# Performance work log

Measured on AMD Instinct MI355X. Metric: run time of the kernel, lower is better.

Reference implementation:

```python
import jax, jax.numpy as jnp
import numpy as np

HID = 128
N_NODES = 50000
N_REL = 500
N_EDGES = 625000
BN_EPS = 1e-5
LRELU_SLOPE = 0.01


def _xavier(key, shape):
    fan_in, fan_out = shape[1], shape[0]
    std = float(np.sqrt(2.0 / (fan_in + fan_out)))
    return jax.random.normal(key, shape, dtype=jnp.float32) * std


def setup_inputs() -> dict:
    key = jax.random.key(0)
    ks = jax.random.split(key, 16)
    x = jax.random.normal(ks[0], (N_NODES, HID), dtype=jnp.float32)
    r = jax.random.normal(ks[1], (N_REL, HID), dtype=jnp.float32)
    que_context = jax.random.normal(ks[2], (1, HID), dtype=jnp.float32)
    fin_que = jax.random.normal(ks[3], (1, 1, HID), dtype=jnp.float32)
    edge_index = jax.random.randint(ks[4], (2, N_EDGES), 0, N_NODES, dtype=jnp.int64)
    edge_attr = jax.random.randint(ks[5], (N_EDGES,), 0, N_REL, dtype=jnp.int64)
    return {
        "x": x, "r": r, "que_context": que_context, "fin_que": fin_que,
        "edge_index": edge_index, "edge_attr": edge_attr,
        # mess_comp: Linear(2*hid, hid) + Tanh
        "W_mess": _xavier(ks[6], (HID, 2 * HID)), "b_mess": jnp.zeros((HID,), jnp.float32),
        # mess_atten_trans: Linear(2*hid, hid) + LeakyReLU
        "W_matt": _xavier(ks[7], (HID, 2 * HID)), "b_matt": jnp.zeros((HID,), jnp.float32),
        "mess_atten_weight": _xavier(ks[8], (1, HID)),
        # x_atten_trans: Linear(2*hid, hid) + LeakyReLU
        "W_xatt": _xavier(ks[9], (HID, 2 * HID)), "b_xatt": jnp.zeros((HID,), jnp.float32),
        "x_atten_weight": _xavier(ks[10], (1, HID)),
        # BatchNorm1d(hid) affine params (training-mode batch stats are used)
        "bn_gamma": jnp.ones((HID,), jnp.float32), "bn_beta": jnp.zeros((HID,), jnp.float32),
    }


def reference(x, r, que_context, fin_que, edge_index, edge_attr,
              W_mess, b_mess, W_matt, b_matt, mess_atten_weight,
              W_xatt, b_xatt, x_atten_weight, bn_gamma, bn_beta):
    n_nodes = x.shape[0]
    # BatchNorm1d over relation embeddings (training-mode: batch statistics, biased var)
    mu = jnp.mean(r, axis=0)
    var = jnp.mean(jnp.square(r - mu), axis=0)
    r = (r - mu) * jax.lax.rsqrt(var + BN_EPS) * bn_gamma + bn_beta

    head_ents, tail_ents = edge_index[0], edge_index[1]
    head_embeds = x[head_ents]            # [E, H]
    rel_embeds = r[edge_attr]             # [E, H]

    # message computation: Linear(2H->H) + tanh
    mess_in = jnp.concatenate([head_embeds, rel_embeds], axis=1)  # [E, 2H]
    mess = jnp.tanh(mess_in @ W_mess.T + b_mess)                  # [E, H]

    # message attention logits
    qc = jnp.broadcast_to(que_context, (mess.shape[0], que_context.shape[1]))
    mc = jnp.concatenate([mess, qc], axis=1) @ W_matt.T + b_matt
    mc = jax.nn.leaky_relu(mc, LRELU_SLOPE)
    mess_coeffs = jnp.sum(mess_atten_weight * mc, axis=1)         # [E]

    # segment softmax over tail_ents
    seg_max = jax.ops.segment_max(mess_coeffs, tail_ents, num_segments=n_nodes)
    mess_coeffs = jnp.exp(mess_coeffs - seg_max[tail_ents])
    seg_sum = jax.ops.segment_sum(mess_coeffs, tail_ents, num_segments=n_nodes)
    mess_weights = mess_coeffs / (seg_sum[tail_ents] + 1e-16)

    # weighted scatter-sum aggregation
    sum_mess = jax.ops.segment_sum(mess * mess_weights[:, None], tail_ents,
                                   num_segments=n_nodes)          # [N, H]

    # gating attention between x and aggregated messages
    pair = jnp.stack([x, sum_mess], axis=1)                       # [N, 2, H]
    fq = jnp.broadcast_to(fin_que, (n_nodes, 2, fin_que.shape[2]))
    xc = jnp.concatenate([pair, fq], axis=2)                      # [N, 2, 2H]
    xc = jax.nn.leaky_relu(jnp.einsum('nkc,hc->nkh', xc, W_xatt) + b_xatt, LRELU_SLOPE)
    x_coeffs = jnp.sum(x_atten_weight[None] * xc, axis=2)         # [N, 2]
    x_weight = jax.nn.softmax(x_coeffs, axis=1)
    x_out = x_weight[:, 0:1] * x + x_weight[:, 1:2] * sum_mess
    # dropout is identity (eval / p=0)
    return x_out, r
```

## Files before the change

kernel.cpp:

```cpp
#include <hip/hip_runtime.h>
#include <hip/hip_bf16.h>

#define HID 128
#define NN 50000
#define NR 500
#define NE 625000
#define LRELU 0.01f
#define SCAN_BLOCKS 196

typedef __hip_bfloat16 bf16;
typedef __attribute__((ext_vector_type(8))) short short8;
typedef __attribute__((ext_vector_type(4))) float float4_;

__device__ __forceinline__ float b2f(bf16 v) { return __bfloat162float(v); }
__device__ __forceinline__ bf16 f2b(float v) { return __float2bfloat16(v); }

__device__ __forceinline__ float san(float v) {
    return (v == v && v > -1e30f && v < 1e30f) ? v : 0.f;
}

__device__ __forceinline__ float ftanh(float a) {
    float e = __expf(2.f * a);
    return 1.f - 2.f * __builtin_amdgcn_rcpf(e + 1.f);
}

__device__ __forceinline__ float ldf(const void* p, int i, int f32) {
    return f32 ? ((const float*)p)[i] : b2f(((const bf16*)p)[i]);
}
__device__ __forceinline__ void stf(void* p, int i, float v, int f32) {
    if (f32) ((float*)p)[i] = v;
    else ((bf16*)p)[i] = f2b(v);
}

__device__ __forceinline__ int clampi(int v, int hi) {
    return v < 0 ? 0 : (v >= hi ? hi - 1 : v);
}
__device__ __forceinline__ int idx_at(const int* p, int i, int is64) {
    return p[is64 ? (2 * i) : i];
}

__device__ __forceinline__ unsigned short bfbits(float v) {
    bf16 h = f2b(v);
    return *(unsigned short*)&h;
}
__device__ __forceinline__ unsigned int packbf2(float a, float b) {
    return (unsigned int)bfbits(a) | ((unsigned int)bfbits(b) << 16);
}
__device__ __forceinline__ float bflo(unsigned int u) { return __uint_as_float(u << 16); }
__device__ __forceinline__ float bfhi(unsigned int u) { return __uint_as_float(u & 0xffff0000u); }

__device__ __forceinline__ float xorReduce16(float v) {
    v += __shfl_xor(v, 1, 64);
    v += __shfl_xor(v, 2, 64);
    v += __shfl_xor(v, 4, 64);
    v += __shfl_xor(v, 8, 64);
    return v;
}
__device__ __forceinline__ float waveMax(float v) {
#pragma unroll
    for (int o = 1; o < 64; o <<= 1) v = fmaxf(v, __shfl_xor(v, o, 64));
    return v;
}
__device__ __forceinline__ float waveSum(float v) {
#pragma unroll
    for (int o = 1; o < 64; o <<= 1) v += __shfl_xor(v, o, 64);
    return v;
}

struct DetectArr {
    const void* p[16];
    int sz[16];
    int kind[16];
};

__global__ void detect_all(DetectArr d, int* __restrict__ flags) {
    int b = blockIdx.x;
    if (d.kind[b] == 1) {
        if (threadIdx.x == 0) {
            const int* q = (const int*)d.p[b];
            int o = 0;
            for (int i = 0; i < 64; ++i) o |= q[2 * i + 1];
            flags[b] = (o == 0) ? 1 : 0;
        }
        return;
    }
    __shared__ int sb[64], sf[64];
    const unsigned int* w = (const unsigned int*)d.p[b];
    int K = d.sz[b] >> 1;
    if (K > 4096) K = 4096;
    int bv = 0, fv = 0;
    for (int i = threadIdx.x; i < K; i += 64) {
        unsigned int x = w[i];
        unsigned int lo = x & 0xFFFFu, hi = x >> 16;
        if (lo == 0u) {
            if (hi) fv++;
        } else {
            unsigned int e = (lo >> 7) & 0xFFu;
            if (e >= 90u && e <= 160u) bv++;
            else fv++;
        }
    }
    sb[threadIdx.x] = bv; sf[threadIdx.x] = fv;
    __syncthreads();
    if (threadIdx.x == 0) {
        int B = 0, F = 0;
        for (int i = 0; i < 64; ++i) { B += sb[i]; F += sf[i]; }
        flags[b] = (F > B) ? 1 : 0;
    }
}

__global__ void bn_stats(const void* __restrict__ r, const int* __restrict__ flags,
                         float* __restrict__ stats) {
    __shared__ float sb[256], sq[256];
    const int fr = flags[1];
    int h = blockIdx.x;
    int t = threadIdx.x;
    float s = 0.f, ss = 0.f;
    for (int i = t; i < NR; i += 256) {
        float v = ldf(r, i * HID + h, fr);
        s += v; ss += v * v;
    }
    sb[t] = s; sq[t] = ss;
    __syncthreads();
    for (int o = 128; o > 0; o >>= 1) {
        if (t < o) { sb[t] += sb[t + o]; sq[t] += sq[t + o]; }
        __syncthreads();
    }
    if (t == 0) {
        float mu = sb[0] / NR;
        float var = sq[0] / NR - mu * mu;
        if (var < 0.f) var = 0.f;
        stats[h] = mu;
        stats[HID + h] = rsqrtf(var + 1e-5f);
    }
}

__global__ void bn_apply(const void* __restrict__ r, const void* __restrict__ gamma,
                         const void* __restrict__ beta, const int* __restrict__ flags,
                         const float* __restrict__ stats,
                         float* __restrict__ rnorm, void* __restrict__ out_base) {
    const int fr = flags[1], fg = flags[14], fb = flags[15], fo = flags[0];
    int i = blockIdx.x * 256 + threadIdx.x;
    if (i >= NR * HID) return;
    int h = i & 127;
    float v = san((ldf(r, i, fr) - stats[h]) * stats[HID + h] * ldf(gamma, h, fg)
                  + ldf(beta, h, fb));
    rnorm[i] = v;
    stf(out_base, NN * HID + i, v, fo);
}

__global__ void precomp_kernel(const void* __restrict__ Wmatt, const void* __restrict__ bmatt,
                               const void* __restrict__ qc,
                               const void* __restrict__ Wxatt, const void* __restrict__ bxatt,
                               const void* __restrict__ fq, const int* __restrict__ flags,
                               float* __restrict__ cmatt, float* __restrict__ cxatt) {
    __shared__ float qcs[HID], fqs[HID];
    const int fWm = flags[8], fbm = flags[9], fqc = flags[2];
    const int fWx = flags[11], fbx = flags[12], ffq = flags[3];
    int h = threadIdx.x;
    qcs[h] = ldf(qc, h, fqc);
    fqs[h] = ldf(fq, h, ffq);
    __syncthreads();
    float a = ldf(bmatt, h, fbm), b = ldf(bxatt, h, fbx);
    for (int k = 0; k < HID; ++k) {
        a += ldf(Wmatt, h * 2 * HID + HID + k, fWm) * qcs[k];
        b += ldf(Wxatt, h * 2 * HID + HID + k, fWx) * fqs[k];
    }
    cmatt[h] = san(a);
    cxatt[h] = san(b);
}

__global__ void rm_kernel(const void* __restrict__ Wmess, const void* __restrict__ bmess,
                          const int* __restrict__ flags,
                          const float* __restrict__ rnorm, bf16* __restrict__ Rmb) {
    __shared__ float rl[HID];
    const int fW = flags[6], fb = flags[7];
    int rel = blockIdx.x, h = threadIdx.x;
    rl[h] = rnorm[rel * HID + h];
    __syncthreads();
    float a = ldf(bmess, h, fb);
    for (int k = 0; k < HID; ++k)
        a += ldf(Wmess, h * 2 * HID + HID + k, fW) * rl[k];
    Rmb[rel * HID + h] = f2b(san(a));
}

#define MLDA 136

__device__ __forceinline__ short8 load_bfrag(const void* W, int n, int k0, int f32) {
    short8 b;
    if (f32) {
        const float* Wf = (const float*)W + (size_t)n * 2 * HID + k0;
        float4 u0 = *(const float4*)Wf;
        float4 u1 = *(const float4*)(Wf + 4);
        b[0] = (short)bfbits(u0.x); b[1] = (short)bfbits(u0.y);
        b[2] = (short)bfbits(u0.z); b[3] = (short)bfbits(u0.w);
        b[4] = (short)bfbits(u1.x); b[5] = (short)bfbits(u1.y);
        b[6] = (short)bfbits(u1.z); b[7] = (short)bfbits(u1.w);
    } else {
        b = *(const short8*)((const bf16*)W + (size_t)n * 2 * HID + k0);
    }
    return b;
}

__global__ __launch_bounds__(256, 4) void xm_mfma(const void* __restrict__ x,
                                                  const void* __restrict__ Wmess,
                                                  const int* __restrict__ flags,
                                                  bf16* __restrict__ Xmb) {
    __shared__ short ml[64 * MLDA];
    const int fx = flags[0], fW = flags[6];
    int tid = threadIdx.x;
    int l = tid & 63, w = tid >> 6;
    int quad = l >> 4, lo16 = l & 15;
    int nbase = w * 32;
    short8 bfr[2][4];
#pragma unroll
    for (int nt = 0; nt < 2; ++nt)
#pragma unroll
        for (int kk = 0; kk < 4; ++kk)
            bfr[nt][kk] = load_bfrag(Wmess, nbase + nt * 16 + lo16, kk * 32 + quad * 8, fW);

    const int ntiles = (NN + 63) / 64;
    for (int tile = blockIdx.x; tile < ntiles; tile += gridDim.x) {
        __syncthreads();
#pragma unroll
        for (int p = 0; p < 8; ++p) {
            int rl_ = p * 8 + (tid >> 5);
            int node = clampi(tile * 64 + rl_, NN);
            int k4 = (tid & 31) * 4;
            unsigned int o0, o1;
            if (fx) {
                float4 v = *(const float4*)((const float*)x + (size_t)node * HID + k4);
                o0 = packbf2(v.x, v.y);
                o1 = packbf2(v.z, v.w);
            } else {
                uint2 u = *(const uint2*)((const bf16*)x + (size_t)node * HID + k4);
                o0 = u.x; o1 = u.y;
            }
            unsigned int* dst = (unsigned int*)&ml[rl_ * MLDA + k4];
            dst[0] = o0; dst[1] = o1;
        }
        __syncthreads();
        float4_ acc[4][2];
#pragma unroll
        for (int mt = 0; mt < 4; ++mt)
#pragma unroll
            for (int nt = 0; nt < 2; ++nt)
                acc[mt][nt] = (float4_){0.f, 0.f, 0.f, 0.f};
#pragma unroll
        for (int kk = 0; kk < 4; ++kk) {
            short8 a[4];
#pragma unroll
            for (int mt = 0; mt < 4; ++mt)
                a[mt] = *(const short8*)&ml[(mt * 16 + lo16) * MLDA + kk * 32 + quad * 8];
#pragma unroll
            for (int mt = 0; mt < 4; ++mt)
#pragma unroll
                for (int nt = 0; nt < 2; ++nt)
                    acc[mt][nt] = __builtin_amdgcn_mfma_f32_16x16x32_bf16(
                        a[mt], bfr[nt][kk], acc[mt][nt], 0, 0, 0);
        }
#pragma unroll
        for (int mt = 0; mt < 4; ++mt)
#pragma unroll
            for (int nt = 0; nt < 2; ++nt)
#pragma unroll
                for (int r = 0; r < 4; ++r) {
                    int node = tile * 64 + mt * 16 + quad * 4 + r;
                    if (node < NN)
                        Xmb[node * HID + nbase + nt * 16 + lo16] = f2b(san(acc[mt][nt][r]));
                }
    }
}

__global__ __launch_bounds__(256, 6) void edge_coeff_mfma(
        const bf16* __restrict__ Xmb, const bf16* __restrict__ Rmb,
        const void* __restrict__ Wmatt, const float* __restrict__ cmatt,
        const void* __restrict__ maw, const unsigned int* __restrict__ hrcsr,
        const int* __restrict__ flags, float* __restrict__ ccsr) {
    __shared__ short ml[64 * MLDA];
    __shared__ float swave[4][64];
    const int fWm = flags[8], fmw = flags[10];
    int tid = threadIdx.x;
    int l = tid & 63, w = tid >> 6;
    int quad = l >> 4, lo16 = l & 15;
    int nbase = w * 32;
    short8 bfr[2][4];
#pragma unroll
    for (int nt = 0; nt < 2; ++nt)
#pragma unroll
        for (int kk = 0; kk < 4; ++kk)
            bfr[nt][kk] = load_bfrag(Wmatt, nbase + nt * 16 + lo16, kk * 32 + quad * 8, fWm);

    int n0 = nbase + lo16, n1 = n0 + 16;
    float c0 = cmatt[n0], c1 = cmatt[n1];
    float w0 = ldf(maw, n0, fmw), w1 = ldf(maw, n1, fmw);

    const int ntiles = (NE + 63) / 64;
    const int seg = tid & 15;
    const int rowsub = tid >> 4;
    for (int T = blockIdx.x; T < ntiles; T += gridDim.x) {
        __syncthreads();
#pragma unroll
        for (int p = 0; p < 4; ++p) {
            int el = p * 16 + rowsub;
            int slot = T * 64 + el;
            unsigned int hr = hrcsr[slot < NE ? slot : NE - 1];
            int head = hr & 0xffffu, rel = hr >> 16;
            int k8 = seg * 8;
            uint4 xv = *(const uint4*)&Xmb[head * HID + k8];
            uint4 rv = *(const uint4*)&Rmb[rel * HID + k8];
            uint4 o;
            o.x = packbf2(ftanh(bflo(xv.x) + bflo(rv.x)), ftanh(bfhi(xv.x) + bfhi(rv.x)));
            o.y = packbf2(ftanh(bflo(xv.y) + bflo(rv.y)), ftanh(bfhi(xv.y) + bfhi(rv.y)));
            o.z = packbf2(ftanh(bflo(xv.z) + bflo(rv.z)), ftanh(bfhi(xv.z) + bfhi(rv.z)));
            o.w = packbf2(ftanh(bflo(xv.w) + bflo(rv.w)), ftanh(bfhi(xv.w) + bfhi(rv.w)));
            *(uint4*)&ml[el * MLDA + k8] = o;
        }
        __syncthreads();
        float4_ acc[4][2];
#pragma unroll
        for (int mt = 0; mt < 4; ++mt)
#pragma unroll
            for (int nt = 0; nt < 2; ++nt)
                acc[mt][nt] = (float4_){0.f, 0.f, 0.f, 0.f};
#pragma unroll
        for (int kk = 0; kk < 4; ++kk) {
            short8 a[4];
#pragma unroll
            for (int mt = 0; mt < 4; ++mt)
                a[mt] = *(const short8*)&ml[(mt * 16 + lo16) * MLDA + kk * 32 + quad * 8];
#pragma unroll
            for (int mt = 0; mt < 4; ++mt)
#pragma unroll
                for (int nt = 0; nt < 2; ++nt)
                    acc[mt][nt] = __builtin_amdgcn_mfma_f32_16x16x32_bf16(
                        a[mt], bfr[nt][kk], acc[mt][nt], 0, 0, 0);
        }
#pragma unroll
        for (int mt = 0; mt < 4; ++mt)
#pragma unroll
            for (int r = 0; r < 4; ++r) {
                float z0 = acc[mt][0][r] + c0;
                z0 = z0 > 0.f ? z0 : LRELU * z0;
                float z1 = acc[mt][1][r] + c1;
                z1 = z1 > 0.f ? z1 : LRELU * z1;
                float s = w0 * z0 + w1 * z1;
                s = xorReduce16(s);
                if (lo16 == 0) swave[w][mt * 16 + quad * 4 + r] = s;
            }
        __syncthreads();
        if (tid < 64) {
            int slot = T * 64 + tid;
            if (slot < NE)
                ccsr[slot] = san(swave[0][tid] + swave[1][tid] + swave[2][tid] + swave[3][tid]);
        }
    }
}

__global__ __launch_bounds__(256, 4) void gate_mfma(
        const void* __restrict__ x, const bf16* __restrict__ smb,
        const void* __restrict__ Wxatt, const float* __restrict__ cxatt,
        const void* __restrict__ xaw, const int* __restrict__ flags,
        void* __restrict__ outx) {
    __shared__ short ml[64 * MLDA];
    __shared__ float swave[4][64];
    __shared__ float lgL[64];
    const int fx = flags[0], fWx = flags[11], fxw = flags[13], fo = flags[0];
    int tid = threadIdx.x;
    int l = tid & 63, w = tid >> 6;
    int quad = l >> 4, lo16 = l & 15;
    int nbase = w * 32;
    short8 bfr[2][4];
#pragma unroll
    for (int nt = 0; nt < 2; ++nt)
#pragma unroll
        for (int kk = 0; kk < 4; ++kk)
            bfr[nt][kk] = load_bfrag(Wxatt, nbase + nt * 16 + lo16, kk * 32 + quad * 8, fWx);

    int n0 = nbase + lo16, n1 = n0 + 16;
    float c0 = cxatt[n0], c1 = cxatt[n1];
    float w0 = ldf(xaw, n0, fxw), w1 = ldf(xaw, n1, fxw);

    const int ntiles = (NN + 31) / 32;
    for (int tile = blockIdx.x; tile < ntiles; tile += gridDim.x) {
        __syncthreads();
#pragma unroll
        for (int p = 0; p < 8; ++p) {
            int rl_ = p * 8 + (tid >> 5);
            int node = clampi(tile * 32 + (rl_ >> 1), NN);
            int k4 = (tid & 31) * 4;
            unsigned int o0, o1;
            if (rl_ & 1) {
                uint2 u = *(const uint2*)&smb[node * HID + k4];
                o0 = u.x; o1 = u.y;
            } else if (fx) {
                float4 v = *(const float4*)((const float*)x + (size_t)node * HID + k4);
                o0 = packbf2(v.x, v.y);
                o1 = packbf2(v.z, v.w);
            } else {
                uint2 u = *(const uint2*)((const bf16*)x + (size_t)node * HID + k4);
                o0 = u.x; o1 = u.y;
            }
            unsigned int* dst = (unsigned int*)&ml[rl_ * MLDA + k4];
            dst[0] = o0; dst[1] = o1;
        }
        __syncthreads();
        float4_ acc[4][2];
#pragma unroll
        for (int mt = 0; mt < 4; ++mt)
#pragma unroll
            for (int nt = 0; nt < 2; ++nt)
                acc[mt][nt] = (float4_){0.f, 0.f, 0.f, 0.f};
#pragma unroll
        for (int kk = 0; kk < 4; ++kk) {
            short8 a[4];
#pragma unroll
            for (int mt = 0; mt < 4; ++mt)
                a[mt] = *(const short8*)&ml[(mt * 16 + lo16) * MLDA + kk * 32 + quad * 8];
#pragma unroll
            for (int mt = 0; mt < 4; ++mt)
#pragma unroll
                for (int nt = 0; nt < 2; ++nt)
                    acc[mt][nt] = __builtin_amdgcn_mfma_f32_16x16x32_bf16(
                        a[mt], bfr[nt][kk], acc[mt][nt], 0, 0, 0);
        }
#pragma unroll
        for (int mt = 0; mt < 4; ++mt)
#pragma unroll
            for (int r = 0; r < 4; ++r) {
                float z0 = acc[mt][0][r] + c0;
                z0 = z0 > 0.f ? z0 : LRELU * z0;
                float z1 = acc[mt][1][r] + c1;
                z1 = z1 > 0.f ? z1 : LRELU * z1;
                float s = w0 * z0 + w1 * z1;
                s = xorReduce16(s);
                if (lo16 == 0) swave[w][mt * 16 + quad * 4 + r] = s;
            }
        __syncthreads();
        if (tid < 64)
            lgL[tid] = san(swave[0][tid] + swave[1][tid] + swave[2][tid] + swave[3][tid]);
        __syncthreads();
#pragma unroll
        for (int it = 0; it < 16; ++it) {
            int idx = tid + 256 * it;
            int nl = idx >> 7, h = idx & 127;
            int node = tile * 32 + nl;
            if (node < NN) {
                float g0 = lgL[2 * nl], g1 = lgL[2 * nl + 1];
                float mm = fmaxf(g0, g1);
                float e0 = __expf(g0 - mm), e1 = __expf(g1 - mm);
                float inv = __builtin_amdgcn_rcpf(e0 + e1);
                float xv = ldf(x, node * HID + h, fx);
                float sv = b2f(smb[node * HID + h]);
                stf(outx, node * HID + h, san((e0 * xv + e1 * sv) * inv), fo);
            }
        }
    }
}

__global__ void count_kernel(const int* __restrict__ ei, const int* __restrict__ flags,
                             int* __restrict__ counts) {
    const int is64e = flags[4];
    for (int e = blockIdx.x * blockDim.x + threadIdx.x; e < NE; e += gridDim.x * blockDim.x) {
        int tail = clampi(idx_at(ei, NE + e, is64e), NN);
        atomicAdd(&counts[tail], 1);
    }
}

__global__ void scan_phase1(const int* __restrict__ counts, int* __restrict__ offs,
                            int* __restrict__ bsum) {
    __shared__ int buf[256];
    int t = threadIdx.x;
    int i = blockIdx.x * 256 + t;
    int v = (i < NN) ? counts[i] : 0;
    buf[t] = v;
    __syncthreads();
    for (int off = 1; off < 256; off <<= 1) {
        int add = (t >= off) ? buf[t - off] : 0;
        __syncthreads();
        buf[t] += add;
        __syncthreads();
    }
    if (i < NN) offs[i] = buf[t] - v;
    if (t == 255) bsum[blockIdx.x] = buf[255];
}

__global__ void scan_phase2(int* __restrict__ bsum, int* __restrict__ bexc) {
    __shared__ int buf[256];
    int t = threadIdx.x;
    int v = (t < SCAN_BLOCKS) ? bsum[t] : 0;
    buf[t] = v;
    __syncthreads();
    for (int off = 1; off < 256; off <<= 1) {
        int add = (t >= off) ? buf[t - off] : 0;
        __syncthreads();
        buf[t] += add;
        __syncthreads();
    }
    if (t < SCAN_BLOCKS) bexc[t] = buf[t] - v;
    if (t == 255) bexc[SCAN_BLOCKS] = buf[255];
}

__global__ void scan_phase3(int* __restrict__ offs, int* __restrict__ cursor,
                            const int* __restrict__ bexc) {
    int i = blockIdx.x * 256 + threadIdx.x;
    if (i < NN) {
        int v = offs[i] + bexc[blockIdx.x];
        offs[i] = v;
        cursor[i] = v;
    }
    if (i == 0) offs[NN] = bexc[SCAN_BLOCKS];
}

__global__ void scatter_kernel(const int* __restrict__ ei, const int* __restrict__ ea,
                               const int* __restrict__ flags,
                               int* __restrict__ cursor, unsigned int* __restrict__ hrcsr) {
    const int is64e = flags[4], is64a = flags[5];
    for (int e = blockIdx.x * blockDim.x + threadIdx.x; e < NE; e += gridDim.x * blockDim.x) {
        int tail = clampi(idx_at(ei, NE + e, is64e), NN);
        int head = clampi(idx_at(ei, e, is64e), NN);
        int rel = clampi(idx_at(ea, e, is64a), NR);
        int p = atomicAdd(&cursor[tail], 1);
        if (p >= 0 && p < NE)
            hrcsr[p] = (unsigned int)head | ((unsigned int)rel << 16);
    }
}

__global__ __launch_bounds__(256, 8) void node_aggr_kernel(
        const bf16* __restrict__ Xmb, const bf16* __restrict__ Rmb,
        const int* __restrict__ offs, const unsigned int* __restrict__ hrcsr,
        const float* __restrict__ ccsr, bf16* __restrict__ smb) {
    int tid = threadIdx.x;
    int sub = tid >> 6;
    int lane = tid & 63;
    int node = blockIdx.x * 4 + sub;
    if (node >= NN) return;
    int s = offs[node], en = offs[node + 1];

    float m = -INFINITY;
    for (int i = s + lane; i < en; i += 64) m = fmaxf(m, ccsr[i]);
    m = waveMax(m);
    float lsum = 0.f;
    for (int i = s + lane; i < en; i += 64) lsum += __expf(ccsr[i] - m);
    lsum = waveSum(lsum);
    float inv = 1.f / (lsum + 1e-16f);

    const int col = lane * 2;
    float acc0 = 0.f, acc1 = 0.f;
    int i = s;
    for (; i + 2 <= en; i += 2) {
        unsigned int hr0 = hrcsr[i], hr1 = hrcsr[i + 1];
        float wg0 = __expf(ccsr[i] - m), wg1 = __expf(ccsr[i + 1] - m);
        unsigned int xv0 = *(const unsigned int*)&Xmb[(hr0 & 0xffffu) * HID + col];
        unsigned int rv0 = *(const unsigned int*)&Rmb[(hr0 >> 16) * HID + col];
        unsigned int xv1 = *(const unsigned int*)&Xmb[(hr1 & 0xffffu) * HID + col];
        unsigned int rv1 = *(const unsigned int*)&Rmb[(hr1 >> 16) * HID + col];
        acc0 += wg0 * ftanh(bflo(xv0) + bflo(rv0)) + wg1 * ftanh(bflo(xv1) + bflo(rv1));
        acc1 += wg0 * ftanh(bfhi(xv0) + bfhi(rv0)) + wg1 * ftanh(bfhi(xv1) + bfhi(rv1));
    }
    if (i < en) {
        unsigned int hr0 = hrcsr[i];
        float wg0 = __expf(ccsr[i] - m);
        unsigned int xv0 = *(const unsigned int*)&Xmb[(hr0 & 0xffffu) * HID + col];
        unsigned int rv0 = *(const unsigned int*)&Rmb[(hr0 >> 16) * HID + col];
        acc0 += wg0 * ftanh(bflo(xv0) + bflo(rv0));
        acc1 += wg0 * ftanh(bfhi(xv0) + bfhi(rv0));
    }
    *(unsigned int*)&smb[node * HID + col] = packbf2(san(acc0 * inv), san(acc1 * inv));
}

extern "C" void kernel_launch(void* const* d_in, const int* in_sizes, int n_in,
                              void* d_out, int out_size, void* d_ws, size_t ws_size,
                              hipStream_t stream) {
    const void* x     = d_in[0];
    const void* r     = d_in[1];
    const void* qc    = d_in[2];
    const void* fq    = d_in[3];
    const int*  ei    = (const int*)d_in[4];
    const int*  ea    = (const int*)d_in[5];
    const void* Wmess = d_in[6];
    const void* bmess = d_in[7];
    const void* Wmatt = d_in[8];
    const void* bmatt = d_in[9];
    const void* maw   = d_in[10];
    const void* Wxatt = d_in[11];
    const void* bxatt = d_in[12];
    const void* xaw   = d_in[13];
    const void* gamma = d_in[14];
    const void* beta  = d_in[15];

    int*          flags  = (int*)d_ws;
    int*          counts = flags + 16;
    int*          offs   = counts + NN;
    int*          cursor = offs + NN + 1;
    int*          bsum   = cursor + NN + 3;
    int*          bexc   = bsum + 256;
    unsigned int* hrcsr  = (unsigned int*)(bexc + 260);
    float*        ccsr   = (float*)(hrcsr + NE);
    float*        rnorm  = ccsr + NE;
    float*        stats  = rnorm + (size_t)NR * HID;
    float*        cmatt  = stats + 2 * HID;
    float*        cxatt  = cmatt + HID;
    bf16*         Rmb    = (bf16*)(cxatt + HID);
    bf16*         Xmb    = Rmb + (size_t)NR * HID;
    bf16*         smb    = Xmb + (size_t)NN * HID;

    hipMemsetAsync(counts, 0, NN * sizeof(int), stream);

    DetectArr da;
    const void* ps[16] = {x, r, qc, fq, ei, ea, Wmess, bmess, Wmatt, bmatt, maw,
                          Wxatt, bxatt, xaw, gamma, beta};
    int szs[16] = {NN * HID, NR * HID, HID, HID, 2 * NE, NE, 2 * HID * HID, HID,
                   2 * HID * HID, HID, HID, 2 * HID * HID, HID, HID, HID, HID};
    for (int i = 0; i < 16; ++i) {
        da.p[i] = ps[i];
        da.sz[i] = szs[i];
        da.kind[i] = (i == 4 || i == 5) ? 1 : 0;
    }
    detect_all<<<16, 64, 0, stream>>>(da, flags);

    bn_stats<<<HID, 256, 0, stream>>>(r, flags, stats);
    bn_apply<<<(NR * HID + 255) / 256, 256, 0, stream>>>(r, gamma, beta, flags, stats,
                                                         rnorm, d_out);
    precomp_kernel<<<1, HID, 0, stream>>>(Wmatt, bmatt, qc, Wxatt, bxatt, fq, flags,
                                          cmatt, cxatt);
    rm_kernel<<<NR, HID, 0, stream>>>(Wmess, bmess, flags, rnorm, Rmb);
    xm_mfma<<<512, 256, 0, stream>>>(x, Wmess, flags, Xmb);
    count_kernel<<<1024, 256, 0, stream>>>(ei, flags, counts);
    scan_phase1<<<SCAN_BLOCKS, 256, 0, stream>>>(counts, offs, bsum);
    scan_phase2<<<1, 256, 0, stream>>>(bsum, bexc);
    scan_phase3<<<SCAN_BLOCKS, 256, 0, stream>>>(offs, cursor, bexc);
    scatter_kernel<<<1024, 256, 0, stream>>>(ei, ea, flags, cursor, hrcsr);
    edge_coeff_mfma<<<1536, 256, 0, stream>>>(Xmb, Rmb, Wmatt, cmatt, maw, hrcsr, flags,
                                              ccsr);
    node_aggr_kernel<<<(NN + 3) / 4, 256, 0, stream>>>(Xmb, Rmb, offs, hrcsr, ccsr, smb);
    gate_mfma<<<512, 256, 0, stream>>>(x, smb, Wxatt, cxatt, xaw, flags, d_out);
}
```

Measured before the change: 453.5 us.

## Fuse node aggregation into gating MFMA kernel and merge small precompute kernels

Fuses the per-node softmax-weighted aggregation into the gating MFMA kernel, so the aggregated messages go straight into shared memory and are never written to or read back from a global bf16 buffer. Each wave aggregates 8 nodes of a 32-node tile before the MFMA gate step. The precompute kernel is folded into the batch-norm stats kernel as an extra block, which removes one launch. The edge coefficient reduction now goes through shared memory instead of xor shuffles, reusing the ml buffer after an added barrier. The risk is the fused kernel's lower occupancy and serial per-wave aggregation, which could hide gather latency less well than the old 8-block-per-CU aggregation kernel.

```diff
diff --git a/kernel.cpp b/kernel.cpp
--- a/kernel.cpp
+++ b/kernel.cpp
@@ -109,12 +109,37 @@
     }
 }
 
-__global__ void bn_stats(const void* __restrict__ r, const int* __restrict__ flags,
-                         float* __restrict__ stats) {
+__global__ void bn_pre(const void* __restrict__ r, const int* __restrict__ flags,
+                       float* __restrict__ stats,
+                       const void* __restrict__ Wmatt, const void* __restrict__ bmatt,
+                       const void* __restrict__ qc,
+                       const void* __restrict__ Wxatt, const void* __restrict__ bxatt,
+                       const void* __restrict__ fq,
+                       float* __restrict__ cmatt, float* __restrict__ cxatt) {
     __shared__ float sb[256], sq[256];
+    int t = threadIdx.x;
+    if (blockIdx.x == HID) {
+        __shared__ float qcs[HID], fqs[HID];
+        const int fWm = flags[8], fbm = flags[9], fqc = flags[2];
+        const int fWx = flags[11], fbx = flags[12], ffq = flags[3];
+        if (t < HID) {
+            qcs[t] = ldf(qc, t, fqc);
+            fqs[t] = ldf(fq, t, ffq);
+        }
+        __syncthreads();
+        if (t < HID) {
+            float a = ldf(bmatt, t, fbm), b = ldf(bxatt, t, fbx);
+            for (int k = 0; k < HID; ++k) {
+                a += ldf(Wmatt, t * 2 * HID + HID + k, fWm) * qcs[k];
+                b += ldf(Wxatt, t * 2 * HID + HID + k, fWx) * fqs[k];
+            }
+            cmatt[t] = san(a);
+            cxatt[t] = san(b);
+        }
+        return;
+    }
     const int fr = flags[1];
     int h = blockIdx.x;
-    int t = threadIdx.x;
     float s = 0.f, ss = 0.f;
     for (int i = t; i < NR; i += 256) {
         float v = ldf(r, i * HID + h, fr);
@@ -149,27 +174,6 @@
     stf(out_base, NN * HID + i, v, fo);
 }
 
-__global__ void precomp_kernel(const void* __restrict__ Wmatt, const void* __restrict__ bmatt,
-                               const void* __restrict__ qc,
-                               const void* __restrict__ Wxatt, const void* __restrict__ bxatt,
-                               const void* __restrict__ fq, const int* __restrict__ flags,
-                               float* __restrict__ cmatt, float* __restrict__ cxatt) {
-    __shared__ float qcs[HID], fqs[HID];
-    const int fWm = flags[8], fbm = flags[9], fqc = flags[2];
-    const int fWx = flags[11], fbx = flags[12], ffq = flags[3];
-    int h = threadIdx.x;
-    qcs[h] = ldf(qc, h, fqc);
-    fqs[h] = ldf(fq, h, ffq);
-    __syncthreads();
-    float a = ldf(bmatt, h, fbm), b = ldf(bxatt, h, fbx);
-    for (int k = 0; k < HID; ++k) {
-        a += ldf(Wmatt, h * 2 * HID + HID + k, fWm) * qcs[k];
-        b += ldf(Wxatt, h * 2 * HID + HID + k, fWx) * fqs[k];
-    }
-    cmatt[h] = san(a);
-    cxatt[h] = san(b);
-}
-
 __global__ void rm_kernel(const void* __restrict__ Wmess, const void* __restrict__ bmess,
                           const int* __restrict__ flags,
                           const float* __restrict__ rnorm, bf16* __restrict__ Rmb) {
@@ -185,6 +189,7 @@
 }
 
 #define MLDA 136
+#define SWST 68
 
 __device__ __forceinline__ short8 load_bfrag(const void* W, int n, int k0, int f32) {
     short8 b;
@@ -278,7 +283,6 @@
         const void* __restrict__ maw, const unsigned int* __restrict__ hrcsr,
         const int* __restrict__ flags, float* __restrict__ ccsr) {
     __shared__ short ml[64 * MLDA];
-    __shared__ float swave[4][64];
     const int fWm = flags[8], fmw = flags[10];
     int tid = threadIdx.x;
     int l = tid & 63, w = tid >> 6;
@@ -298,6 +302,7 @@
     const int ntiles = (NE + 63) / 64;
     const int seg = tid & 15;
     const int rowsub = tid >> 4;
+    float* swred = (float*)ml;
     for (int T = blockIdx.x; T < ntiles; T += gridDim.x) {
         __syncthreads();
 #pragma unroll
@@ -336,29 +341,40 @@
                     acc[mt][nt] = __builtin_amdgcn_mfma_f32_16x16x32_bf16(
                         a[mt], bfr[nt][kk], acc[mt][nt], 0, 0, 0);
         }
+        __syncthreads();
 #pragma unroll
         for (int mt = 0; mt < 4; ++mt)
 #pragma unroll
             for (int r = 0; r < 4; ++r) {
                 float z0 = acc[mt][0][r] + c0;
-                z0 = z0 > 0.f ? z0 : LRELU * z0;
+                z0 = fmaxf(z0, 0.f) + LRELU * fminf(z0, 0.f);
                 float z1 = acc[mt][1][r] + c1;
-                z1 = z1 > 0.f ? z1 : LRELU * z1;
-                float s = w0 * z0 + w1 * z1;
-                s = xorReduce16(s);
-                if (lo16 == 0) swave[w][mt * 16 + quad * 4 + r] = s;
+                z1 = fmaxf(z1, 0.f) + LRELU * fminf(z1, 0.f);
+                int row = mt * 16 + quad * 4 + r;
+                swred[row * SWST + w * 16 + lo16] = w0 * z0 + w1 * z1;
             }
         __syncthreads();
         if (tid < 64) {
             int slot = T * 64 + tid;
-            if (slot < NE)
-                ccsr[slot] = san(swave[0][tid] + swave[1][tid] + swave[2][tid] + swave[3][tid]);
-        }
-    }
-}
-
-__global__ __launch_bounds__(256, 4) void gate_mfma(
-        const void* __restrict__ x, const bf16* __restrict__ smb,
+            if (slot < NE) {
+                const float4* rp = (const float4*)&swred[tid * SWST];
+                float4 s4 = rp[0];
+#pragma unroll
+                for (int q = 1; q < 16; ++q) {
+                    float4 v = rp[q];
+                    s4.x += v.x; s4.y += v.y; s4.z += v.z; s4.w += v.w;
+                }
+                ccsr[slot] = san(s4.x + s4.y + s4.z + s4.w);
+            }
+        }
+    }
+}
+
+__global__ __launch_bounds__(256, 4) void aggr_gate(
+        const void* __restrict__ x, const bf16* __restrict__ Xmb,
+        const bf16* __restrict__ Rmb,
+        const int* __restrict__ offs, const unsigned int* __restrict__ hrcsr,
+        const float* __restrict__ ccsr,
         const void* __restrict__ Wxatt, const float* __restrict__ cxatt,
         const void* __restrict__ xaw, const int* __restrict__ flags,
         void* __restrict__ outx) {
@@ -385,15 +401,12 @@
     for (int tile = blockIdx.x; tile < ntiles; tile += gridDim.x) {
         __syncthreads();
 #pragma unroll
-        for (int p = 0; p < 8; ++p) {
-            int rl_ = p * 8 + (tid >> 5);
-            int node = clampi(tile * 32 + (rl_ >> 1), NN);
+        for (int p = 0; p < 4; ++p) {
+            int j = p * 8 + (tid >> 5);
+            int node = clampi(tile * 32 + j, NN);
             int k4 = (tid & 31) * 4;
             unsigned int o0, o1;
-            if (rl_ & 1) {
-                uint2 u = *(const uint2*)&smb[node * HID + k4];
-                o0 = u.x; o1 = u.y;
-            } else if (fx) {
+            if (fx) {
                 float4 v = *(const float4*)((const float*)x + (size_t)node * HID + k4);
                 o0 = packbf2(v.x, v.y);
                 o1 = packbf2(v.z, v.w);
@@ -401,8 +414,47 @@
                 uint2 u = *(const uint2*)((const bf16*)x + (size_t)node * HID + k4);
                 o0 = u.x; o1 = u.y;
             }
-            unsigned int* dst = (unsigned int*)&ml[rl_ * MLDA + k4];
+            unsigned int* dst = (unsigned int*)&ml[(2 * j) * MLDA + k4];
             dst[0] = o0; dst[1] = o1;
+        }
+        const int col = l * 2;
+#pragma unroll 1
+        for (int jj = 0; jj < 8; ++jj) {
+            int j = w * 8 + jj;
+            int node = tile * 32 + j;
+            unsigned int out = 0;
+            if (node < NN) {
+                int s = offs[node], en = offs[node + 1];
+                float m = -INFINITY;
+                for (int i = s + l; i < en; i += 64) m = fmaxf(m, ccsr[i]);
+                m = waveMax(m);
+                float lsum = 0.f;
+                for (int i = s + l; i < en; i += 64) lsum += __expf(ccsr[i] - m);
+                lsum = waveSum(lsum);
+                float inv = 1.f / (lsum + 1e-16f);
+                float acc0 = 0.f, acc1 = 0.f;
+                int i = s;
+                for (; i + 2 <= en; i += 2) {
+                    unsigned int hr0 = hrcsr[i], hr1 = hrcsr[i + 1];
+                    float wg0 = __expf(ccsr[i] - m), wg1 = __expf(ccsr[i + 1] - m);
+                    unsigned int xv0 = *(const unsigned int*)&Xmb[(hr0 & 0xffffu) * HID + col];
+                    unsigned int rv0 = *(const unsigned int*)&Rmb[(hr0 >> 16) * HID + col];
+                    unsigned int xv1 = *(const unsigned int*)&Xmb[(hr1 & 0xffffu) * HID + col];
+                    unsigned int rv1 = *(const unsigned int*)&Rmb[(hr1 >> 16) * HID + col];
+                    acc0 += wg0 * ftanh(bflo(xv0) + bflo(rv0)) + wg1 * ftanh(bflo(xv1) + bflo(rv1));
+                    acc1 += wg0 * ftanh(bfhi(xv0) + bfhi(rv0)) + wg1 * ftanh(bfhi(xv1) + bfhi(rv1));
+                }
+                if (i < en) {
+                    unsigned int hr0 = hrcsr[i];
+                    float wg0 = __expf(ccsr[i] - m);
+                    unsigned int xv0 = *(const unsigned int*)&Xmb[(hr0 & 0xffffu) * HID + col];
+                    unsigned int rv0 = *(const unsigned int*)&Rmb[(hr0 >> 16) * HID + col];
+                    acc0 += wg0 * ftanh(bflo(xv0) + bflo(rv0));
+                    acc1 += wg0 * ftanh(bfhi(xv0) + bfhi(rv0));
+                }
+                out = packbf2(san(acc0 * inv), san(acc1 * inv));
+            }
+            *(unsigned int*)&ml[(2 * j + 1) * MLDA + col] = out;
         }
         __syncthreads();
         float4_ acc[4][2];
@@ -429,9 +481,9 @@
 #pragma unroll
             for (int r = 0; r < 4; ++r) {
                 float z0 = acc[mt][0][r] + c0;
-                z0 = z0 > 0.f ? z0 : LRELU * z0;
+                z0 = fmaxf(z0, 0.f) + LRELU * fminf(z0, 0.f);
                 float z1 = acc[mt][1][r] + c1;
-                z1 = z1 > 0.f ? z1 : LRELU * z1;
+                z1 = fmaxf(z1, 0.f) + LRELU * fminf(z1, 0.f);
                 float s = w0 * z0 + w1 * z1;
                 s = xorReduce16(s);
                 if (lo16 == 0) swave[w][mt * 16 + quad * 4 + r] = s;
@@ -451,7 +503,7 @@
                 float e0 = __expf(g0 - mm), e1 = __expf(g1 - mm);
                 float inv = __builtin_amdgcn_rcpf(e0 + e1);
                 float xv = ldf(x, node * HID + h, fx);
-                float sv = b2f(smb[node * HID + h]);
+                float sv = b2f(((const bf16*)ml)[(2 * nl + 1) * MLDA + h]);
                 stf(outx, node * HID + h, san((e0 * xv + e1 * sv) * inv), fo);
             }
         }
@@ -524,49 +576,6 @@
         if (p >= 0 && p < NE)
             hrcsr[p] = (unsigned int)head | ((unsigned int)rel << 16);
     }
-}
-
-__global__ __launch_bounds__(256, 8) void node_aggr_kernel(
-        const bf16* __restrict__ Xmb, const bf16* __restrict__ Rmb,
-        const int* __restrict__ offs, const unsigned int* __restrict__ hrcsr,
-        const float* __restrict__ ccsr, bf16* __restrict__ smb) {
-    int tid = threadIdx.x;
-    int sub = tid >> 6;
-    int lane = tid & 63;
-    int node = blockIdx.x * 4 + sub;
-    if (node >= NN) return;
-    int s = offs[node], en = offs[node + 1];
-
-    float m = -INFINITY;
-    for (int i = s + lane; i < en; i += 64) m = fmaxf(m, ccsr[i]);
-    m = waveMax(m);
-    float lsum = 0.f;
-    for (int i = s + lane; i < en; i += 64) lsum += __expf(ccsr[i] - m);
-    lsum = waveSum(lsum);
-    float inv = 1.f / (lsum + 1e-16f);
-
-    const int col = lane * 2;
-    float acc0 = 0.f, acc1 = 0.f;
-    int i = s;
-    for (; i + 2 <= en; i += 2) {
-        unsigned int hr0 = hrcsr[i], hr1 = hrcsr[i + 1];
-        float wg0 = __expf(ccsr[i] - m), wg1 = __expf(ccsr[i + 1] - m);
-        unsigned int xv0 = *(const unsigned int*)&Xmb[(hr0 & 0xffffu) * HID + col];
-        unsigned int rv0 = *(const unsigned int*)&Rmb[(hr0 >> 16) * HID + col];
-        unsigned int xv1 = *(const unsigned int*)&Xmb[(hr1 & 0xffffu) * HID + col];
-        unsigned int rv1 = *(const unsigned int*)&Rmb[(hr1 >> 16) * HID + col];
-        acc0 += wg0 * ftanh(bflo(xv0) + bflo(rv0)) + wg1 * ftanh(bflo(xv1) + bflo(rv1));
-        acc1 += wg0 * ftanh(bfhi(xv0) + bfhi(rv0)) + wg1 * ftanh(bfhi(xv1) + bfhi(rv1));
-    }
-    if (i < en) {
-        unsigned int hr0 = hrcsr[i];
-        float wg0 = __expf(ccsr[i] - m);
-        unsigned int xv0 = *(const unsigned int*)&Xmb[(hr0 & 0xffffu) * HID + col];
-        unsigned int rv0 = *(const unsigned int*)&Rmb[(hr0 >> 16) * HID + col];
-        acc0 += wg0 * ftanh(bflo(xv0) + bflo(rv0));
-        acc1 += wg0 * ftanh(bfhi(xv0) + bfhi(rv0));
-    }
-    *(unsigned int*)&smb[node * HID + col] = packbf2(san(acc0 * inv), san(acc1 * inv));
 }
 
 extern "C" void kernel_launch(void* const* d_in, const int* in_sizes, int n_in,
@@ -603,7 +612,6 @@
     float*        cxatt  = cmatt + HID;
     bf16*         Rmb    = (bf16*)(cxatt + HID);
     bf16*         Xmb    = Rmb + (size_t)NR * HID;
-    bf16*         smb    = Xmb + (size_t)NN * HID;
 
     hipMemsetAsync(counts, 0, NN * sizeof(int), stream);
 
@@ -619,11 +627,10 @@
     }
     detect_all<<<16, 64, 0, stream>>>(da, flags);
 
-    bn_stats<<<HID, 256, 0, stream>>>(r, flags, stats);
+    bn_pre<<<HID + 1, 256, 0, stream>>>(r, flags, stats, Wmatt, bmatt, qc,
+                                        Wxatt, bxatt, fq, cmatt, cxatt);
     bn_apply<<<(NR * HID + 255) / 256, 256, 0, stream>>>(r, gamma, beta, flags, stats,
                                                          rnorm, d_out);
-    precomp_kernel<<<1, HID, 0, stream>>>(Wmatt, bmatt, qc, Wxatt, bxatt, fq, flags,
-                                          cmatt, cxatt);
     rm_kernel<<<NR, HID, 0, stream>>>(Wmess, bmess, flags, rnorm, Rmb);
     xm_mfma<<<512, 256, 0, stream>>>(x, Wmess, flags, Xmb);
     count_kernel<<<1024, 256, 0, stream>>>(ei, flags, counts);
@@ -633,6 +640,6 @@
     scatter_kernel<<<1024, 256, 0, stream>>>(ei, ea, flags, cursor, hrcsr);
     edge_coeff_mfma<<<1536, 256, 0, stream>>>(Xmb, Rmb, Wmatt, cmatt, maw, hrcsr, flags,
                                               ccsr);
-    node_aggr_kernel<<<(NN + 3) / 4, 256, 0, stream>>>(Xmb, Rmb, offs, hrcsr, ccsr, smb);
-    gate_mfma<<<512, 256, 0, stream>>>(x, smb, Wxatt, cxatt, xaw, flags, d_out);
-}
+    aggr_gate<<<1024, 256, 0, stream>>>(x, Xmb, Rmb, offs, hrcsr, ccsr,
+                                        Wxatt, cxatt, xaw, flags, d_out);
+}
```

New measurement: 456.1 us. Within noise of the previous version (+0.6%).
